# Performance work log

Measured on AMD Instinct MI355X. Metric: run time of the kernel, lower is better.

Reference implementation:

```python
import jax, jax.numpy as jnp
import numpy as np

B, S, HIDDEN = 4, 2048, 1024
NUM_EXPERTS = 8
TOP_K = 4
EPS = 1e-6


def setup_inputs() -> dict:
    key = jax.random.key(0)
    k0, k1, k2 = jax.random.split(key, 3)
    x = jax.random.normal(k0, (B, S, HIDDEN), dtype=jnp.float32)
    Wg = jax.random.normal(k1, (HIDDEN, NUM_EXPERTS), dtype=jnp.float32) * 0.02
    bg = jnp.zeros((NUM_EXPERTS,), dtype=jnp.float32)
    W = jax.random.normal(k2, (NUM_EXPERTS, HIDDEN, HIDDEN), dtype=jnp.float32) * 0.02
    b = jnp.zeros((NUM_EXPERTS, HIDDEN), dtype=jnp.float32)
    return {"x": x, "Wg": Wg, "bg": bg, "W": W, "b": b}


def reference(x, Wg, bg, W, b):
    Bb, Ss, D = x.shape
    xf = x.reshape(-1, D)                       # [T, D]
    T = xf.shape[0]

    # --- router ---
    router_logits = xf @ Wg + bg                # [T, E]
    router_probs = jax.nn.softmax(router_logits, axis=-1)
    top_k_probs, top_k_indices = jax.lax.top_k(router_probs, TOP_K)  # [T, K]
    top_k_weights = top_k_probs / (top_k_probs.sum(axis=-1, keepdims=True) + EPS)
    expert_mask = jax.nn.one_hot(top_k_indices, NUM_EXPERTS, dtype=jnp.float32).sum(axis=1)  # [T, E]

    # --- experts: original computes every expert on every token then masks;
    # same math expressed as one batched GEMM + gather ---
    all_out = jnp.einsum('td,edf->etf', xf, W) + b[:, None, :]  # [E, T, D]
    sel = all_out[top_k_indices.T, jnp.arange(T)[None, :]]      # [K, T, D]
    moe_output = jnp.einsum('tk,ktd->td', top_k_weights, sel).reshape(Bb, Ss, D)

    # --- load-balancing aux loss ---
    aux_loss = jnp.dot(expert_mask.mean(axis=0), router_probs.mean(axis=0)) * NUM_EXPERTS
    return moe_output, aux_loss
```

## Files before the change

kernel.cpp:

```cpp
#include <hip/hip_runtime.h>
#include <hip/hip_bf16.h>

#define T_TOK 8192
#define DH    1024
#define NE    8
#define TK    4

typedef unsigned short u16;
typedef __bf16 bf16x8 __attribute__((ext_vector_type(8)));
typedef float  f32x4  __attribute__((ext_vector_type(4)));

__device__ __forceinline__ u16 f2b(float f) {
    union { float f; unsigned u; } v; v.f = f;
    unsigned u = v.u;
    u += 0x7FFFu + ((u >> 16) & 1u);
    return (u16)(u >> 16);
}
__device__ __forceinline__ float b2f(u16 h) {
    union { unsigned u; float f; } v; v.u = ((unsigned)h) << 16;
    return v.f;
}
__device__ __forceinline__ void glds16(const u16* g, u16* l) {
    __builtin_amdgcn_global_load_lds((const __attribute__((address_space(1))) void*)g,
                                     (__attribute__((address_space(3))) void*)l, 16, 0, 0);
}

#define FENCE() asm volatile("" ::: "memory")
#define SBAR()  do { FENCE(); __builtin_amdgcn_s_barrier(); FENCE(); } while (0)
#define WAITLGKM0() do { asm volatile("s_waitcnt lgkmcnt(0)" ::: "memory"); \
                         __builtin_amdgcn_sched_barrier(0); } while (0)
#define WAITVM(n) asm volatile("s_waitcnt vmcnt(" #n ")" ::: "memory")

__global__ __launch_bounds__(256) void cast_w_kernel(const float* __restrict__ W,
                                                     u16* __restrict__ wbt,
                                                     int* __restrict__ cnt) {
    __shared__ float tile[64][65];
    if (blockIdx.x == 0 && blockIdx.y == 0 && blockIdx.z == 0 && threadIdx.x < 16)
        cnt[threadIdx.x] = 0;
    const int e  = blockIdx.z;
    const int d0 = blockIdx.y * 64;
    const int f0 = blockIdx.x * 64;
    const int r  = threadIdx.x >> 4;
    const int c4 = (threadIdx.x & 15) * 4;
    const float* src = W + ((size_t)e << 20) + (size_t)d0 * DH + f0;
    #pragma unroll
    for (int i = 0; i < 4; i++) {
        const int row = i * 16 + r;
        const float4 v = *(const float4*)(src + (size_t)row * DH + c4);
        tile[row][c4]     = v.x;
        tile[row][c4 + 1] = v.y;
        tile[row][c4 + 2] = v.z;
        tile[row][c4 + 3] = v.w;
    }
    __syncthreads();
    u16* dst = wbt + ((size_t)e << 20) + (size_t)f0 * DH + d0;
    #pragma unroll
    for (int i = 0; i < 4; i++) {
        const int orow = i * 16 + r;
        ushort4 o;
        o.x = f2b(tile[c4][orow]);
        o.y = f2b(tile[c4 + 1][orow]);
        o.z = f2b(tile[c4 + 2][orow]);
        o.w = f2b(tile[c4 + 3][orow]);
        *(ushort4*)(dst + (size_t)orow * DH + c4) = o;
    }
}

__global__ __launch_bounds__(512) void router_kernel(
    const float* __restrict__ x, const float* __restrict__ Wg, const float* __restrict__ bg,
    u16* __restrict__ xb,
    int* __restrict__ bucket_tok, float* __restrict__ bucket_w,
    int* __restrict__ tk_e, float* __restrict__ tk_w,
    int* __restrict__ cnt, float* __restrict__ probsum)
{
    __shared__ int   lcnt[NE];
    __shared__ float lprob[NE];
    __shared__ int   gbase[NE];
    const int tid = threadIdx.x;
    const int wv = tid >> 6, lane = tid & 63;
    const int t = blockIdx.x * 8 + wv;
    if (tid < NE) { lcnt[tid] = 0; lprob[tid] = 0.f; }
    __syncthreads();

    float a[NE] = {};
    {
        const float* xr = x + (size_t)t * DH;
        u16* xbr = xb + (size_t)t * DH;
        const float4* wg = (const float4*)Wg;
        #pragma unroll
        for (int it = 0; it < 4; it++) {
            const int d = it * 256 + lane * 4;
            const float4 v = *(const float4*)(xr + d);
            ushort4 o;
            o.x = f2b(v.x); o.y = f2b(v.y); o.z = f2b(v.z); o.w = f2b(v.w);
            *(ushort4*)(xbr + d) = o;
            const float4 w0l = wg[2 * (d + 0)], w0h = wg[2 * (d + 0) + 1];
            const float4 w1l = wg[2 * (d + 1)], w1h = wg[2 * (d + 1) + 1];
            const float4 w2l = wg[2 * (d + 2)], w2h = wg[2 * (d + 2) + 1];
            const float4 w3l = wg[2 * (d + 3)], w3h = wg[2 * (d + 3) + 1];
            a[0] += v.x * w0l.x + v.y * w1l.x + v.z * w2l.x + v.w * w3l.x;
            a[1] += v.x * w0l.y + v.y * w1l.y + v.z * w2l.y + v.w * w3l.y;
            a[2] += v.x * w0l.z + v.y * w1l.z + v.z * w2l.z + v.w * w3l.z;
            a[3] += v.x * w0l.w + v.y * w1l.w + v.z * w2l.w + v.w * w3l.w;
            a[4] += v.x * w0h.x + v.y * w1h.x + v.z * w2h.x + v.w * w3h.x;
            a[5] += v.x * w0h.y + v.y * w1h.y + v.z * w2h.y + v.w * w3h.y;
            a[6] += v.x * w0h.z + v.y * w1h.z + v.z * w2h.z + v.w * w3h.z;
            a[7] += v.x * w0h.w + v.y * w1h.w + v.z * w2h.w + v.w * w3h.w;
        }
    }
    #pragma unroll
    for (int e = 0; e < NE; e++) {
        float v = a[e];
        #pragma unroll
        for (int off = 32; off > 0; off >>= 1) v += __shfl_down(v, off);
        a[e] = v;
    }

    int idx4[TK]; float w4[TK]; int off4[TK];
    if (lane == 0) {
        float logits[NE], probs[NE];
        float mx = -1e30f;
        #pragma unroll
        for (int e = 0; e < NE; e++) { logits[e] = a[e] + bg[e]; mx = fmaxf(mx, logits[e]); }
        float Z = 0.f;
        #pragma unroll
        for (int e = 0; e < NE; e++) { probs[e] = expf(logits[e] - mx); Z += probs[e]; }
        const float rZ = 1.f / Z;
        #pragma unroll
        for (int e = 0; e < NE; e++) probs[e] *= rZ;

        float rem2[NE];
        #pragma unroll
        for (int e = 0; e < NE; e++) rem2[e] = probs[e];
        float s4 = 0.f;
        #pragma unroll
        for (int k = 0; k < TK; k++) {
            int best = 0; float bv = rem2[0];
            #pragma unroll
            for (int e = 1; e < NE; e++) if (rem2[e] > bv) { bv = rem2[e]; best = e; }
            idx4[k] = best; w4[k] = bv; s4 += bv; rem2[best] = -1e30f;
        }
        const float rs = 1.f / (s4 + 1e-6f);
        #pragma unroll
        for (int k = 0; k < TK; k++) {
            w4[k] *= rs;
            tk_e[t * TK + k] = idx4[k];
            tk_w[t * TK + k] = w4[k];
            off4[k] = atomicAdd(&lcnt[idx4[k]], 1);
        }
        #pragma unroll
        for (int e = 0; e < NE; e++) atomicAdd(&lprob[e], probs[e]);
    }
    __syncthreads();
    if (tid < NE) {
        gbase[tid] = atomicAdd(&cnt[tid], lcnt[tid]);
        atomicAdd(&probsum[tid], lprob[tid]);
    }
    __syncthreads();
    if (lane == 0) {
        #pragma unroll
        for (int k = 0; k < TK; k++) {
            const int e = idx4[k];
            const int slot = gbase[e] + off4[k];
            bucket_tok[e * T_TOK + slot] = (t << 2) | k;
            bucket_w[e * T_TOK + slot]   = w4[k];
        }
    }
}

__global__ __launch_bounds__(512, 2) void moe_gemm_kernel(
    const u16* __restrict__ xb, const u16* __restrict__ wbt,
    const int* __restrict__ bucket_tok, const float* __restrict__ bucket_w,
    const int* __restrict__ cnt, u16* __restrict__ y)
{
    __shared__ u16 As[2][256 * 64];
    __shared__ u16 Bs[2][256 * 64];
    __shared__ int   s_tok[256];
    __shared__ float s_w[256];

    const int tid  = threadIdx.x;
    const int lane = tid & 63;
    const int wid  = tid >> 6;
    const int wr   = wid >> 2;
    const int wc   = wid & 3;
    const int fr   = lane & 15;
    const int fq   = (lane >> 4) * 8;
    const int swz  = (fr & 7) << 3;
    const int gsw  = ((lane & 7) ^ (lane >> 3)) * 8;
    const int crow = lane >> 3;

    const int ALb = 2 * wid + (wid >= 4 ? 8 : 0);
    const int AHb = ALb + 8;
    const int BLb = (wid >> 1) * 8 + (wid & 1) * 2;
    const int BHb = BLb + 4;

    const int e = blockIdx.x & 7;
    const int c = blockIdx.x >> 3;
    const int M = cnt[e];

    for (int j = 0; j < 4; ++j) {
        const int idx = j * 32 + c;
        const int mb = idx >> 2;
        const int nb = idx & 3;
        const int m0 = mb << 8;
        if (m0 >= M) continue;
        const int n0 = nb << 8;
        const int mrows = M - m0;
        const bool active = (mrows > 128) || (wr == 0);

        __syncthreads();
        if (tid < 256) {
            const int slot = m0 + tid;
            if (slot < M) {
                s_tok[tid] = bucket_tok[e * T_TOK + slot];
                s_w[tid]   = bucket_w[e * T_TOK + slot];
            } else { s_tok[tid] = -1; s_w[tid] = 0.f; }
        }
        __syncthreads();

        const int rAL0 = ALb * 8 + crow, rAL1 = rAL0 + 8;
        const int rAH0 = AHb * 8 + crow, rAH1 = rAH0 + 8;
        const int tAL0 = s_tok[rAL0], tAL1 = s_tok[rAL1];
        const int tAH0 = s_tok[rAH0], tAH1 = s_tok[rAH1];
        const u16* gAL0 = xb + (size_t)(tAL0 >= 0 ? (tAL0 >> 2) : 0) * DH + gsw;
        const u16* gAL1 = xb + (size_t)(tAL1 >= 0 ? (tAL1 >> 2) : 0) * DH + gsw;
        const u16* gAH0 = xb + (size_t)(tAH0 >= 0 ? (tAH0 >> 2) : 0) * DH + gsw;
        const u16* gAH1 = xb + (size_t)(tAH1 >= 0 ? (tAH1 >> 2) : 0) * DH + gsw;
        const u16* wbe  = wbt + ((size_t)e << 20);
        const u16* gBL0 = wbe + (size_t)(n0 + BLb * 8 + crow) * DH + gsw;
        const u16* gBL1 = gBL0 + (size_t)8 * DH;
        const u16* gBH0 = wbe + (size_t)(n0 + BHb * 8 + crow) * DH + gsw;
        const u16* gBH1 = gBH0 + (size_t)8 * DH;

        f32x4 acc[8][4] = {};

        #pragma unroll
        for (int kt = 0; kt < 2; kt++) {
            const int ko = kt * 64; const int p = kt;
            glds16(gAL0 + ko, &As[p][ALb * 512]); glds16(gAL1 + ko, &As[p][(ALb + 1) * 512]);
            glds16(gAH0 + ko, &As[p][AHb * 512]); glds16(gAH1 + ko, &As[p][(AHb + 1) * 512]);
            glds16(gBL0 + ko, &Bs[p][BLb * 512]); glds16(gBL1 + ko, &Bs[p][(BLb + 1) * 512]);
            glds16(gBH0 + ko, &Bs[p][BHb * 512]); glds16(gBH1 + ko, &Bs[p][(BHb + 1) * 512]);
        }
        WAITVM(8);
        SBAR();

        const int arow = (wr * 128 + fr) * 64;
        const int brow = (wc * 64  + fr) * 64;
        const int c0 = fq ^ swz;
        const int c1 = (32 + fq) ^ swz;

        bf16x8 afL[4][2], afH[4][2], bfL[2][2], bfH[2][2];

        for (int kt = 0; kt < 16; ++kt) {
            const int p = kt & 1;
            const u16* Ap = &As[p][0];
            const u16* Bp = &Bs[p][0];

            if (active) {
                #pragma unroll
                for (int mi = 0; mi < 4; mi++) {
                    afL[mi][0] = *(const bf16x8*)&Ap[arow + mi * 1024 + c0];
                    afL[mi][1] = *(const bf16x8*)&Ap[arow + mi * 1024 + c1];
                }
                #pragma unroll
                for (int nj = 0; nj < 2; nj++) {
                    bfL[nj][0] = *(const bf16x8*)&Bp[brow + nj * 1024 + c0];
                    bfL[nj][1] = *(const bf16x8*)&Bp[brow + nj * 1024 + c1];
                }
            }
            if (kt >= 1 && kt <= 14) {
                const int ko = (kt + 1) * 64; const int q = (kt + 1) & 1;
                glds16(gAH0 + ko, &As[q][AHb * 512]);
                glds16(gAH1 + ko, &As[q][(AHb + 1) * 512]);
            }
            asm volatile("s_waitcnt lgkmcnt(8)" ::: "memory");
            SBAR(); WAITLGKM0();
            __builtin_amdgcn_s_setprio(1);
            if (active) {
                #pragma unroll
                for (int mi = 0; mi < 4; mi++)
                    #pragma unroll
                    for (int nj = 0; nj < 2; nj++) {
                        acc[mi][nj] = __builtin_amdgcn_mfma_f32_16x16x32_bf16(afL[mi][0], bfL[nj][0], acc[mi][nj], 0, 0, 0);
                        acc[mi][nj] = __builtin_amdgcn_mfma_f32_16x16x32_bf16(afL[mi][1], bfL[nj][1], acc[mi][nj], 0, 0, 0);
                    }
            }
            __builtin_amdgcn_s_setprio(0);
            SBAR();

            if (active) {
                #pragma unroll
                for (int nj = 0; nj < 2; nj++) {
                    bfH[nj][0] = *(const bf16x8*)&Bp[brow + (nj + 2) * 1024 + c0];
                    bfH[nj][1] = *(const bf16x8*)&Bp[brow + (nj + 2) * 1024 + c1];
                }
            }
            if (kt <= 13) {
                const int ko = (kt + 2) * 64;
                glds16(gAL0 + ko, &As[p][ALb * 512]);
                glds16(gAL1 + ko, &As[p][(ALb + 1) * 512]);
            }
            SBAR(); WAITLGKM0();
            __builtin_amdgcn_s_setprio(1);
            if (active) {
                #pragma unroll
                for (int mi = 0; mi < 4; mi++)
                    #pragma unroll
                    for (int nj = 0; nj < 2; nj++) {
                        acc[mi][nj + 2] = __builtin_amdgcn_mfma_f32_16x16x32_bf16(afL[mi][0], bfH[nj][0], acc[mi][nj + 2], 0, 0, 0);
                        acc[mi][nj + 2] = __builtin_amdgcn_mfma_f32_16x16x32_bf16(afL[mi][1], bfH[nj][1], acc[mi][nj + 2], 0, 0, 0);
                    }
            }
            __builtin_amdgcn_s_setprio(0);
            SBAR();

            if (active) {
                #pragma unroll
                for (int mi = 0; mi < 4; mi++) {
                    afH[mi][0] = *(const bf16x8*)&Ap[arow + (mi + 4) * 1024 + c0];
                    afH[mi][1] = *(const bf16x8*)&Ap[arow + (mi + 4) * 1024 + c1];
                }
            }
            if (kt <= 13) {
                const int ko = (kt + 2) * 64;
                glds16(gBL0 + ko, &Bs[p][BLb * 512]);
                glds16(gBL1 + ko, &Bs[p][(BLb + 1) * 512]);
            }
            SBAR(); WAITLGKM0();
            __builtin_amdgcn_s_setprio(1);
            if (active) {
                #pragma unroll
                for (int mi = 0; mi < 4; mi++)
                    #pragma unroll
                    for (int nj = 0; nj < 2; nj++) {
                        acc[mi + 4][nj + 2] = __builtin_amdgcn_mfma_f32_16x16x32_bf16(afH[mi][0], bfH[nj][0], acc[mi + 4][nj + 2], 0, 0, 0);
                        acc[mi + 4][nj + 2] = __builtin_amdgcn_mfma_f32_16x16x32_bf16(afH[mi][1], bfH[nj][1], acc[mi + 4][nj + 2], 0, 0, 0);
                    }
            }
            __builtin_amdgcn_s_setprio(0);
            SBAR();

            if (kt <= 13) {
                const int ko = (kt + 2) * 64;
                glds16(gBH0 + ko, &Bs[p][BHb * 512]);
                glds16(gBH1 + ko, &Bs[p][(BHb + 1) * 512]);
            }
            __builtin_amdgcn_s_setprio(1);
            if (active) {
                #pragma unroll
                for (int mi = 0; mi < 4; mi++)
                    #pragma unroll
                    for (int nj = 0; nj < 2; nj++) {
                        acc[mi + 4][nj] = __builtin_amdgcn_mfma_f32_16x16x32_bf16(afH[mi][0], bfL[nj][0], acc[mi + 4][nj], 0, 0, 0);
                        acc[mi + 4][nj] = __builtin_amdgcn_mfma_f32_16x16x32_bf16(afH[mi][1], bfL[nj][1], acc[mi + 4][nj], 0, 0, 0);
                    }
            }
            __builtin_amdgcn_s_setprio(0);
            if (kt <= 13)      WAITVM(6);
            else if (kt == 14) WAITVM(0);
            SBAR();
        }

        const int cl = lane & 15;
        const int rb = (lane >> 4) * 4;
        #pragma unroll
        for (int mi = 0; mi < 8; mi++) {
            #pragma unroll
            for (int r = 0; r < 4; r++) {
                const int srow = wr * 128 + mi * 16 + rb + r;
                const int tok = s_tok[srow];
                if (tok < 0) continue;
                const float w = s_w[srow];
                u16* yr = y + (size_t)tok * DH + (n0 + wc * 64 + cl);
                #pragma unroll
                for (int nj = 0; nj < 4; nj++)
                    yr[nj * 16] = f2b(acc[mi][nj][r] * w);
            }
        }
    }
}

__global__ __launch_bounds__(256) void combine_kernel(
    const u16* __restrict__ y, const int* __restrict__ tk_e, const float* __restrict__ tk_w,
    const float* __restrict__ bexp,
    const int* __restrict__ cnt, const float* __restrict__ probsum,
    float* __restrict__ out, float* __restrict__ out_aux)
{
    if (blockIdx.x == 0 && threadIdx.x == 0) {
        float s = 0.f;
        for (int e = 0; e < NE; e++) s += (float)cnt[e] * probsum[e];
        out_aux[0] = s * (float)NE / ((float)T_TOK * (float)T_TOK);
    }
    const int t = blockIdx.x * 2 + (threadIdx.x >> 7);
    const int c = (threadIdx.x & 127) * 8;
    float o[8] = {};
    #pragma unroll
    for (int k = 0; k < TK; k++) {
        const int e   = tk_e[t * TK + k];
        const float w = tk_w[t * TK + k];
        const u16* yp = y + ((size_t)(t * TK + k)) * DH + c;
        const ushort4 y0 = *(const ushort4*)(yp);
        const ushort4 y1 = *(const ushort4*)(yp + 4);
        const float4  b0 = *(const float4*)(bexp + (size_t)e * DH + c);
        const float4  b1 = *(const float4*)(bexp + (size_t)e * DH + c + 4);
        o[0] += b2f(y0.x) + w * b0.x;
        o[1] += b2f(y0.y) + w * b0.y;
        o[2] += b2f(y0.z) + w * b0.z;
        o[3] += b2f(y0.w) + w * b0.w;
        o[4] += b2f(y1.x) + w * b1.x;
        o[5] += b2f(y1.y) + w * b1.y;
        o[6] += b2f(y1.z) + w * b1.z;
        o[7] += b2f(y1.w) + w * b1.w;
    }
    float4 ov0 = {o[0], o[1], o[2], o[3]};
    float4 ov1 = {o[4], o[5], o[6], o[7]};
    *(float4*)(out + (size_t)t * DH + c)     = ov0;
    *(float4*)(out + (size_t)t * DH + c + 4) = ov1;
}

extern "C" void kernel_launch(void* const* d_in, const int* in_sizes, int n_in,
                              void* d_out, int out_size, void* d_ws, size_t ws_size,
                              hipStream_t stream)
{
    const float* x  = (const float*)d_in[0];
    const float* Wg = (const float*)d_in[1];
    const float* bg = (const float*)d_in[2];
    const float* W  = (const float*)d_in[3];
    const float* b  = (const float*)d_in[4];
    float* out = (float*)d_out;

    char* ws = (char*)d_ws;
    u16*   xb         = (u16*)(ws);
    u16*   wbt        = (u16*)(ws + 16777216);
    u16*   y          = (u16*)(ws + 33554432);
    int*   bucket_tok = (int*)(ws + 100663296);
    float* bucket_w   = (float*)(ws + 100925440);
    int*   tk_e       = (int*)(ws + 101187584);
    float* tk_w       = (float*)(ws + 101318656);
    int*   cnt        = (int*)(ws + 101449728);
    float* probsum    = (float*)(ws + 101449760);


    cast_w_kernel<<<dim3(16, 16, NE), 256, 0, stream>>>(W, wbt, cnt);
    router_kernel<<<1024, 512, 0, stream>>>(x, Wg, bg, xb, bucket_tok, bucket_w, tk_e, tk_w, cnt, probsum);
    moe_gemm_kernel<<<dim3(256), 512, 0, stream>>>(xb, wbt, bucket_tok, bucket_w, cnt, y);
    combine_kernel<<<4096, 256, 0, stream>>>(y, tk_e, tk_w, b, cnt, probsum, out, out + (size_t)T_TOK * DH);
}
```

Baseline: 277.1 us.

## Fuse weight cast and router into one prep kernel; drop active-warp gating

Merges the weight transpose/cast kernel and the router kernel into a single launch, where the first 1024 blocks each transpose two 64x64 weight tiles and the remaining blocks run routing. Counter zeroing moves to a hipMemsetAsync. Separately, the GEMM loop no longer skips LDS reads and MFMAs for warps whose rows are beyond the bucket size, which removes branches but does extra work on padded rows. Fusing overlaps the memory-bound cast with routing and removes one launch, at the cost of a larger shared-memory footprint per block that may lower occupancy for the router part.

```diff
diff --git a/kernel.cpp b/kernel.cpp
--- a/kernel.cpp
+++ b/kernel.cpp
@@ -31,54 +31,59 @@
                          __builtin_amdgcn_sched_barrier(0); } while (0)
 #define WAITVM(n) asm volatile("s_waitcnt vmcnt(" #n ")" ::: "memory")
 
-__global__ __launch_bounds__(256) void cast_w_kernel(const float* __restrict__ W,
-                                                     u16* __restrict__ wbt,
-                                                     int* __restrict__ cnt) {
-    __shared__ float tile[64][65];
-    if (blockIdx.x == 0 && blockIdx.y == 0 && blockIdx.z == 0 && threadIdx.x < 16)
-        cnt[threadIdx.x] = 0;
-    const int e  = blockIdx.z;
-    const int d0 = blockIdx.y * 64;
-    const int f0 = blockIdx.x * 64;
-    const int r  = threadIdx.x >> 4;
-    const int c4 = (threadIdx.x & 15) * 4;
-    const float* src = W + ((size_t)e << 20) + (size_t)d0 * DH + f0;
-    #pragma unroll
-    for (int i = 0; i < 4; i++) {
-        const int row = i * 16 + r;
-        const float4 v = *(const float4*)(src + (size_t)row * DH + c4);
-        tile[row][c4]     = v.x;
-        tile[row][c4 + 1] = v.y;
-        tile[row][c4 + 2] = v.z;
-        tile[row][c4 + 3] = v.w;
-    }
-    __syncthreads();
-    u16* dst = wbt + ((size_t)e << 20) + (size_t)f0 * DH + d0;
-    #pragma unroll
-    for (int i = 0; i < 4; i++) {
-        const int orow = i * 16 + r;
-        ushort4 o;
-        o.x = f2b(tile[c4][orow]);
-        o.y = f2b(tile[c4 + 1][orow]);
-        o.z = f2b(tile[c4 + 2][orow]);
-        o.w = f2b(tile[c4 + 3][orow]);
-        *(ushort4*)(dst + (size_t)orow * DH + c4) = o;
-    }
-}
-
-__global__ __launch_bounds__(512) void router_kernel(
+__global__ __launch_bounds__(512) void prep_kernel(
+    const float* __restrict__ W, u16* __restrict__ wbt,
     const float* __restrict__ x, const float* __restrict__ Wg, const float* __restrict__ bg,
     u16* __restrict__ xb,
     int* __restrict__ bucket_tok, float* __restrict__ bucket_w,
     int* __restrict__ tk_e, float* __restrict__ tk_w,
     int* __restrict__ cnt, float* __restrict__ probsum)
 {
+    __shared__ float tile2[2][64][65];
     __shared__ int   lcnt[NE];
     __shared__ float lprob[NE];
     __shared__ int   gbase[NE];
+
+    const int bid = blockIdx.x;
     const int tid = threadIdx.x;
+
+    if (bid < 1024) {
+        const int half = tid >> 8;
+        const int tloc = tid & 255;
+        const int r  = tloc >> 4;
+        const int c4 = (tloc & 15) * 4;
+        float (*tile)[65] = tile2[half];
+        const int jc = bid * 2 + half;
+        const int f0 = (jc & 15) * 64;
+        const int d0 = ((jc >> 4) & 15) * 64;
+        const int e  = jc >> 8;
+        const float* src = W + ((size_t)e << 20) + (size_t)d0 * DH + f0;
+        #pragma unroll
+        for (int i = 0; i < 4; i++) {
+            const int row = i * 16 + r;
+            const float4 v = *(const float4*)(src + (size_t)row * DH + c4);
+            tile[row][c4]     = v.x;
+            tile[row][c4 + 1] = v.y;
+            tile[row][c4 + 2] = v.z;
+            tile[row][c4 + 3] = v.w;
+        }
+        __syncthreads();
+        u16* dst = wbt + ((size_t)e << 20) + (size_t)f0 * DH + d0;
+        #pragma unroll
+        for (int i = 0; i < 4; i++) {
+            const int orow = i * 16 + r;
+            ushort4 o;
+            o.x = f2b(tile[c4][orow]);
+            o.y = f2b(tile[c4 + 1][orow]);
+            o.z = f2b(tile[c4 + 2][orow]);
+            o.w = f2b(tile[c4 + 3][orow]);
+            *(ushort4*)(dst + (size_t)orow * DH + c4) = o;
+        }
+        return;
+    }
+
     const int wv = tid >> 6, lane = tid & 63;
-    const int t = blockIdx.x * 8 + wv;
+    const int t = (bid - 1024) * 8 + wv;
     if (tid < NE) { lcnt[tid] = 0; lprob[tid] = 0.f; }
     __syncthreads();
 
@@ -205,8 +210,6 @@
         const int m0 = mb << 8;
         if (m0 >= M) continue;
         const int n0 = nb << 8;
-        const int mrows = M - m0;
-        const bool active = (mrows > 128) || (wr == 0);
 
         __syncthreads();
         if (tid < 256) {
@@ -257,17 +260,15 @@
             const u16* Ap = &As[p][0];
             const u16* Bp = &Bs[p][0];
 
-            if (active) {
-                #pragma unroll
-                for (int mi = 0; mi < 4; mi++) {
-                    afL[mi][0] = *(const bf16x8*)&Ap[arow + mi * 1024 + c0];
-                    afL[mi][1] = *(const bf16x8*)&Ap[arow + mi * 1024 + c1];
-                }
-                #pragma unroll
-                for (int nj = 0; nj < 2; nj++) {
-                    bfL[nj][0] = *(const bf16x8*)&Bp[brow + nj * 1024 + c0];
-                    bfL[nj][1] = *(const bf16x8*)&Bp[brow + nj * 1024 + c1];
-                }
+            #pragma unroll
+            for (int mi = 0; mi < 4; mi++) {
+                afL[mi][0] = *(const bf16x8*)&Ap[arow + mi * 1024 + c0];
+                afL[mi][1] = *(const bf16x8*)&Ap[arow + mi * 1024 + c1];
+            }
+            #pragma unroll
+            for (int nj = 0; nj < 2; nj++) {
+                bfL[nj][0] = *(const bf16x8*)&Bp[brow + nj * 1024 + c0];
+                bfL[nj][1] = *(const bf16x8*)&Bp[brow + nj * 1024 + c1];
             }
             if (kt >= 1 && kt <= 14) {
                 const int ko = (kt + 1) * 64; const int q = (kt + 1) & 1;
@@ -277,24 +278,20 @@
             asm volatile("s_waitcnt lgkmcnt(8)" ::: "memory");
             SBAR(); WAITLGKM0();
             __builtin_amdgcn_s_setprio(1);
-            if (active) {
+            #pragma unroll
+            for (int mi = 0; mi < 4; mi++)
                 #pragma unroll
-                for (int mi = 0; mi < 4; mi++)
-                    #pragma unroll
-                    for (int nj = 0; nj < 2; nj++) {
-                        acc[mi][nj] = __builtin_amdgcn_mfma_f32_16x16x32_bf16(afL[mi][0], bfL[nj][0], acc[mi][nj], 0, 0, 0);
-                        acc[mi][nj] = __builtin_amdgcn_mfma_f32_16x16x32_bf16(afL[mi][1], bfL[nj][1], acc[mi][nj], 0, 0, 0);
-                    }
-            }
+                for (int nj = 0; nj < 2; nj++) {
+                    acc[mi][nj] = __builtin_amdgcn_mfma_f32_16x16x32_bf16(afL[mi][0], bfL[nj][0], acc[mi][nj], 0, 0, 0);
+                    acc[mi][nj] = __builtin_amdgcn_mfma_f32_16x16x32_bf16(afL[mi][1], bfL[nj][1], acc[mi][nj], 0, 0, 0);
+                }
             __builtin_amdgcn_s_setprio(0);
             SBAR();
 
-            if (active) {
-                #pragma unroll
-                for (int nj = 0; nj < 2; nj++) {
-                    bfH[nj][0] = *(const bf16x8*)&Bp[brow + (nj + 2) * 1024 + c0];
-                    bfH[nj][1] = *(const bf16x8*)&Bp[brow + (nj + 2) * 1024 + c1];
-                }
+            #pragma unroll
+            for (int nj = 0; nj < 2; nj++) {
+                bfH[nj][0] = *(const bf16x8*)&Bp[brow + (nj + 2) * 1024 + c0];
+                bfH[nj][1] = *(const bf16x8*)&Bp[brow + (nj + 2) * 1024 + c1];
             }
             if (kt <= 13) {
                 const int ko = (kt + 2) * 64;
@@ -303,24 +300,20 @@
             }
             SBAR(); WAITLGKM0();
             __builtin_amdgcn_s_setprio(1);
-            if (active) {
+            #pragma unroll
+            for (int mi = 0; mi < 4; mi++)
                 #pragma unroll
-                for (int mi = 0; mi < 4; mi++)
-                    #pragma unroll
-                    for (int nj = 0; nj < 2; nj++) {
-                        acc[mi][nj + 2] = __builtin_amdgcn_mfma_f32_16x16x32_bf16(afL[mi][0], bfH[nj][0], acc[mi][nj + 2], 0, 0, 0);
-                        acc[mi][nj + 2] = __builtin_amdgcn_mfma_f32_16x16x32_bf16(afL[mi][1], bfH[nj][1], acc[mi][nj + 2], 0, 0, 0);
-                    }
-            }
+                for (int nj = 0; nj < 2; nj++) {
+                    acc[mi][nj + 2] = __builtin_amdgcn_mfma_f32_16x16x32_bf16(afL[mi][0], bfH[nj][0], acc[mi][nj + 2], 0, 0, 0);
+                    acc[mi][nj + 2] = __builtin_amdgcn_mfma_f32_16x16x32_bf16(afL[mi][1], bfH[nj][1], acc[mi][nj + 2], 0, 0, 0);
+                }
             __builtin_amdgcn_s_setprio(0);
             SBAR();
 
-            if (active) {
-                #pragma unroll
-                for (int mi = 0; mi < 4; mi++) {
-                    afH[mi][0] = *(const bf16x8*)&Ap[arow + (mi + 4) * 1024 + c0];
-                    afH[mi][1] = *(const bf16x8*)&Ap[arow + (mi + 4) * 1024 + c1];
-                }
+            #pragma unroll
+            for (int mi = 0; mi < 4; mi++) {
+                afH[mi][0] = *(const bf16x8*)&Ap[arow + (mi + 4) * 1024 + c0];
+                afH[mi][1] = *(const bf16x8*)&Ap[arow + (mi + 4) * 1024 + c1];
             }
             if (kt <= 13) {
                 const int ko = (kt + 2) * 64;
@@ -329,15 +322,13 @@
             }
             SBAR(); WAITLGKM0();
             __builtin_amdgcn_s_setprio(1);
-            if (active) {
+            #pragma unroll
+            for (int mi = 0; mi < 4; mi++)
                 #pragma unroll
-                for (int mi = 0; mi < 4; mi++)
-                    #pragma unroll
-                    for (int nj = 0; nj < 2; nj++) {
-                        acc[mi + 4][nj + 2] = __builtin_amdgcn_mfma_f32_16x16x32_bf16(afH[mi][0], bfH[nj][0], acc[mi + 4][nj + 2], 0, 0, 0);
-                        acc[mi + 4][nj + 2] = __builtin_amdgcn_mfma_f32_16x16x32_bf16(afH[mi][1], bfH[nj][1], acc[mi + 4][nj + 2], 0, 0, 0);
-                    }
-            }
+                for (int nj = 0; nj < 2; nj++) {
+                    acc[mi + 4][nj + 2] = __builtin_amdgcn_mfma_f32_16x16x32_bf16(afH[mi][0], bfH[nj][0], acc[mi + 4][nj + 2], 0, 0, 0);
+                    acc[mi + 4][nj + 2] = __builtin_amdgcn_mfma_f32_16x16x32_bf16(afH[mi][1], bfH[nj][1], acc[mi + 4][nj + 2], 0, 0, 0);
+                }
             __builtin_amdgcn_s_setprio(0);
             SBAR();
 
@@ -347,15 +338,13 @@
                 glds16(gBH1 + ko, &Bs[p][(BHb + 1) * 512]);
             }
             __builtin_amdgcn_s_setprio(1);
-            if (active) {
+            #pragma unroll
+            for (int mi = 0; mi < 4; mi++)
                 #pragma unroll
-                for (int mi = 0; mi < 4; mi++)
-                    #pragma unroll
-                    for (int nj = 0; nj < 2; nj++) {
-                        acc[mi + 4][nj] = __builtin_amdgcn_mfma_f32_16x16x32_bf16(afH[mi][0], bfL[nj][0], acc[mi + 4][nj], 0, 0, 0);
-                        acc[mi + 4][nj] = __builtin_amdgcn_mfma_f32_16x16x32_bf16(afH[mi][1], bfL[nj][1], acc[mi + 4][nj], 0, 0, 0);
-                    }
-            }
+                for (int nj = 0; nj < 2; nj++) {
+                    acc[mi + 4][nj] = __builtin_amdgcn_mfma_f32_16x16x32_bf16(afH[mi][0], bfL[nj][0], acc[mi + 4][nj], 0, 0, 0);
+                    acc[mi + 4][nj] = __builtin_amdgcn_mfma_f32_16x16x32_bf16(afH[mi][1], bfL[nj][1], acc[mi + 4][nj], 0, 0, 0);
+                }
             __builtin_amdgcn_s_setprio(0);
             if (kt <= 13)      WAITVM(6);
             else if (kt == 14) WAITVM(0);
@@ -441,9 +430,10 @@
     int*   cnt        = (int*)(ws + 101449728);
     float* probsum    = (float*)(ws + 101449760);
 
-
-    cast_w_kernel<<<dim3(16, 16, NE), 256, 0, stream>>>(W, wbt, cnt);
-    router_kernel<<<1024, 512, 0, stream>>>(x, Wg, bg, xb, bucket_tok, bucket_w, tk_e, tk_w, cnt, probsum);
+    hipMemsetAsync(cnt, 0, 64, stream);
+
+    prep_kernel<<<2048, 512, 0, stream>>>(W, wbt, x, Wg, bg, xb,
+                                          bucket_tok, bucket_w, tk_e, tk_w, cnt, probsum);
     moe_gemm_kernel<<<dim3(256), 512, 0, stream>>>(xb, wbt, bucket_tok, bucket_w, cnt, y);
     combine_kernel<<<4096, 256, 0, stream>>>(y, tk_e, tk_w, b, cnt, probsum, out, out + (size_t)T_TOK * DH);
 }
```

After: 253.4 us. 8.5% less time.
